# Kernel tuning notes

Measured on AMD Instinct MI355X. Metric: run time of the kernel, lower is better.

## Reference

```python
import jax, jax.numpy as jnp
import numpy as np

NUM_SEQS = 32      # decode batch: one new token per sequence
HIDDEN = 4096
H = 32             # query heads
KVH = 8            # kv heads (GQA group = 4)
D = 128            # head_dim
BS = 16            # paged-cache block size (vLLM default)
MAX_BLOCKS = 128   # blocks per sequence -> max context 2048
MAX_CTX = MAX_BLOCKS * BS
NUM_BLOCKS = NUM_SEQS * MAX_BLOCKS  # total physical blocks
ROPE_BASE = 10000.0


def setup_inputs() -> dict:
    key = jax.random.key(0)
    ks = jax.random.split(key, 10)
    s = 0.02
    hidden_states = jax.random.normal(ks[0], (NUM_SEQS, HIDDEN), jnp.float32)
    Wq = jax.random.normal(ks[1], (HIDDEN, H * D), jnp.float32) * s
    Wk = jax.random.normal(ks[2], (HIDDEN, KVH * D), jnp.float32) * s
    Wv = jax.random.normal(ks[3], (HIDDEN, KVH * D), jnp.float32) * s
    Wo = jax.random.normal(ks[4], (H * D, HIDDEN), jnp.float32) * s
    k_cache = jax.random.normal(ks[5], (NUM_BLOCKS, BS, KVH, D), jnp.float32)
    v_cache = jax.random.normal(ks[6], (NUM_BLOCKS, BS, KVH, D), jnp.float32)
    # disjoint, shuffled physical blocks per sequence (non-contiguous paging)
    perm = jax.random.permutation(ks[7], NUM_BLOCKS)
    block_tables = perm.reshape(NUM_SEQS, MAX_BLOCKS).astype(jnp.int32)
    context_lens = jax.random.randint(ks[8], (NUM_SEQS,), 1, MAX_CTX + 1).astype(jnp.int32)
    return dict(hidden_states=hidden_states, Wq=Wq, Wk=Wk, Wv=Wv, Wo=Wo,
                k_cache=k_cache, v_cache=v_cache,
                block_tables=block_tables, context_lens=context_lens)


def _rotate_half(x):
    x1, x2 = jnp.split(x, 2, axis=-1)
    return jnp.concatenate([-x2, x1], axis=-1)


def reference(hidden_states, Wq, Wk, Wv, Wo, k_cache, v_cache, block_tables, context_lens):
    T = hidden_states.shape[0]
    scale = D ** -0.5
    group = H // KVH

    # QKV projections
    q = (hidden_states @ Wq).reshape(T, H, D)
    k = (hidden_states @ Wk).reshape(T, KVH, D)
    v = (hidden_states @ Wv).reshape(T, KVH, D)

    # RoPE at position = context_len - 1 (HF half-split convention)
    pos = (context_lens - 1).astype(jnp.float32)
    inv_freq = 1.0 / (ROPE_BASE ** (jnp.arange(0, D, 2, dtype=jnp.float32) / D))
    freqs = pos[:, None] * inv_freq[None, :]                     # [T, D/2]
    cos = jnp.concatenate([jnp.cos(freqs)] * 2, -1)[:, None, :]  # [T, 1, D]
    sin = jnp.concatenate([jnp.sin(freqs)] * 2, -1)[:, None, :]
    q = q * cos + _rotate_half(q) * sin
    k = k * cos + _rotate_half(k) * sin

    # write new K/V into the paged cache at slot (ctx-1)
    last = context_lens - 1
    blk_idx = last // BS
    slot = last % BS
    phys = block_tables[jnp.arange(T), blk_idx]                  # [T]
    k_cache = k_cache.at[phys, slot].set(k)
    v_cache = v_cache.at[phys, slot].set(v)

    # gather each sequence's pages: [T, S, KVH, D], S = MAX_CTX
    K = k_cache[block_tables].reshape(T, MAX_CTX, KVH, D)
    V = v_cache[block_tables].reshape(T, MAX_CTX, KVH, D)

    # GQA attention, q_len = 1 per sequence
    qg = q.reshape(T, KVH, group, D)
    scores = jnp.einsum('tkgd,tskd->tkgs', qg, K) * scale        # [T, KVH, G, S]
    valid = jnp.arange(MAX_CTX)[None, :] < context_lens[:, None] # [T, S]
    scores = jnp.where(valid[:, None, None, :], scores, -jnp.inf)
    p = jax.nn.softmax(scores, axis=-1)
    out = jnp.einsum('tkgs,tskd->tkgd', p, V).reshape(T, H * D)
    return out @ Wo
```

## Files before the change

### kernel.cpp

```cpp
#include <hip/hip_runtime.h>
#include <math.h>

#define TSEQ 32
#define HID  4096
#define NH   32
#define NKVH 8
#define HD   128
#define NCOL 6144
#define BSZ  16
#define MAXBLK 128
#define CH   256

#define N_PART   (32*32*6144)
#define OFF_Q    (N_PART)
#define OFF_KN   (OFF_Q  + 131072)
#define OFF_VN   (OFF_KN + 32768)
#define OFF_AT   (OFF_VN + 32768)
#define OFF_AP   (OFF_AT + 131072)
#define OFF_TAB  (OFF_AP + 133120)

__global__ __launch_bounds__(256) void rope_table(const int* __restrict__ ctxl,
                                                  float* __restrict__ tab) {
  int idx = blockIdx.x * 256 + threadIdx.x;
  if (idx >= 32 * 64) return;
  int t = idx >> 6, i = idx & 63;
  double pos = (double)(ctxl[t] - 1);
  double inv = exp(-(double)i * (9.210340371976184 / 64.0));
  double f = pos * inv;
  tab[idx * 2]     = (float)cos(f);
  tab[idx * 2 + 1] = (float)sin(f);
}

__global__ __launch_bounds__(256) void qkv_kernel(
    const float* __restrict__ hs, const float* __restrict__ Wq,
    const float* __restrict__ Wk, const float* __restrict__ Wv,
    float* __restrict__ part) {
  const int lane = threadIdx.x & 63;
  const int wu = __builtin_amdgcn_readfirstlane(threadIdx.x >> 6);
  const int col0 = blockIdx.x * 256 + lane * 4;
  const int kc = blockIdx.y;
  const int k0 = kc * 128;
  const float* W; int ldw, jloc;
  if (col0 < 4096)      { W = Wq; ldw = 4096; jloc = col0; }
  else if (col0 < 5120) { W = Wk; ldw = 1024; jloc = col0 - 4096; }
  else                  { W = Wv; ldw = 1024; jloc = col0 - 5120; }
  float4 acc[8];
#pragma unroll
  for (int r = 0; r < 8; ++r) acc[r] = make_float4(0.f, 0.f, 0.f, 0.f);
  const float* wp = W + (size_t)k0 * ldw + jloc;
  const float* hp = hs + (size_t)(wu * 8) * HID + k0;
#pragma unroll 4
  for (int kk = 0; kk < 128; ++kk) {
    float4 w4 = *(const float4*)(wp + (size_t)kk * ldw);
#pragma unroll
    for (int r = 0; r < 8; ++r) {
      float h = hp[r * HID + kk];
      acc[r].x = fmaf(h, w4.x, acc[r].x);
      acc[r].y = fmaf(h, w4.y, acc[r].y);
      acc[r].z = fmaf(h, w4.z, acc[r].z);
      acc[r].w = fmaf(h, w4.w, acc[r].w);
    }
  }
  float* o = part + (size_t)kc * 32 * NCOL + (size_t)(wu * 8) * NCOL + blockIdx.x * 256 + lane * 4;
#pragma unroll
  for (int r = 0; r < 8; ++r) *(float4*)(o + (size_t)r * NCOL) = acc[r];
}

__global__ __launch_bounds__(256) void rope_kernel(
    const float* __restrict__ part, const float* __restrict__ tab,
    float* __restrict__ q, float* __restrict__ kn, float* __restrict__ vn) {
  const int t = blockIdx.x;
  const int col = (blockIdx.y * 256 + threadIdx.x) * 4;
  float4 sum = make_float4(0.f, 0.f, 0.f, 0.f);
  const float* p = part + (size_t)t * NCOL + col;
#pragma unroll
  for (int c = 0; c < 32; ++c) {
    float4 v = *(const float4*)(p + (size_t)c * 32 * NCOL);
    sum.x += v.x; sum.y += v.y; sum.z += v.z; sum.w += v.w;
  }
  __shared__ float lds[1024];
  *(float4*)&lds[threadIdx.x * 4] = sum;
  __syncthreads();
  float out[4] = {sum.x, sum.y, sum.z, sum.w};
  if (col < 5120) {
#pragma unroll
    for (int j = 0; j < 4; ++j) {
      int d = (col + j) & 127;
      int i = d & 63;
      float partner = lds[(threadIdx.x * 4 + j) ^ 64];
      float c0 = tab[(t * 64 + i) * 2];
      float s0 = tab[(t * 64 + i) * 2 + 1];
      out[j] = (d < 64) ? (out[j] * c0 - partner * s0) : (out[j] * c0 + partner * s0);
    }
  }
  float4 o4 = make_float4(out[0], out[1], out[2], out[3]);
  if (col < 4096)      *(float4*)(q  + (size_t)t * 4096 + col) = o4;
  else if (col < 5120) *(float4*)(kn + (size_t)t * 1024 + (col - 4096)) = o4;
  else                 *(float4*)(vn + (size_t)t * 1024 + (col - 5120)) = o4;
}

__global__ __launch_bounds__(256) void attn_kernel(
    const float* __restrict__ kcache, const float* __restrict__ vcache,
    const int* __restrict__ bt, const int* __restrict__ ctxl,
    const float* __restrict__ q, const float* __restrict__ kn,
    const float* __restrict__ vn, float* __restrict__ part) {
  const int t = blockIdx.x, kvh = blockIdx.y, ch = blockIdx.z;
  const int ctx = ctxl[t];
  const int s0 = ch * CH;
  if (s0 >= ctx) return;
  const int ns = min(CH, ctx - s0);
  const int tid = threadIdx.x;
  const int w = tid >> 6, lane = tid & 63;
  const int half = lane >> 5, dl = lane & 31;

  __shared__ float qs[4][128];
  __shared__ int   bts[128];
  __shared__ float sc[4][CH];
  __shared__ float ml[4][2];
  __shared__ float op[4][4][128];

  for (int i = tid; i < 512; i += 256)
    qs[i >> 7][i & 127] = q[((size_t)t * NH + kvh * 4 + (i >> 7)) * HD + (i & 127)];
  for (int i = tid; i < 128; i += 256) bts[i] = bt[t * MAXBLK + i];
  __syncthreads();

  float4 q0 = *(const float4*)(&qs[0][dl * 4]);
  float4 q1 = *(const float4*)(&qs[1][dl * 4]);
  float4 q2 = *(const float4*)(&qs[2][dl * 4]);
  float4 q3 = *(const float4*)(&qs[3][dl * 4]);
  const float* knp = kn + ((size_t)t * NKVH + kvh) * HD;
  const float* vnp = vn + ((size_t)t * NKVH + kvh) * HD;

#pragma unroll 2
  for (int i = 0; i < CH / 8; ++i) {
    int sl = i * 8 + w * 2 + half;
    bool valid = sl < ns;
    float dot0 = 0.f, dot1 = 0.f, dot2 = 0.f, dot3 = 0.f;
    if (valid) {
      int s = s0 + sl;
      const float* kp;
      if (s == ctx - 1) kp = knp;
      else {
        int phys = bts[s >> 4];
        kp = kcache + (((size_t)phys * BSZ + (s & 15)) * NKVH + kvh) * HD;
      }
      float4 k4 = *(const float4*)(kp + dl * 4);
      dot0 = q0.x*k4.x + q0.y*k4.y + q0.z*k4.z + q0.w*k4.w;
      dot1 = q1.x*k4.x + q1.y*k4.y + q1.z*k4.z + q1.w*k4.w;
      dot2 = q2.x*k4.x + q2.y*k4.y + q2.z*k4.z + q2.w*k4.w;
      dot3 = q3.x*k4.x + q3.y*k4.y + q3.z*k4.z + q3.w*k4.w;
    }
#pragma unroll
    for (int m = 1; m < 32; m <<= 1) {
      dot0 += __shfl_xor(dot0, m, 64);
      dot1 += __shfl_xor(dot1, m, 64);
      dot2 += __shfl_xor(dot2, m, 64);
      dot3 += __shfl_xor(dot3, m, 64);
    }
    if (dl == 0) {
      const float scale = 0.08838834764831845f;
      sc[0][sl] = valid ? dot0 * scale : -INFINITY;
      sc[1][sl] = valid ? dot1 * scale : -INFINITY;
      sc[2][sl] = valid ? dot2 * scale : -INFINITY;
      sc[3][sl] = valid ? dot3 * scale : -INFINITY;
    }
  }
  __syncthreads();

  {
    const int g = w;
    float vals[4];
    float m = -INFINITY;
#pragma unroll
    for (int i = 0; i < 4; ++i) { vals[i] = sc[g][lane + i * 64]; m = fmaxf(m, vals[i]); }
#pragma unroll
    for (int mk = 1; mk < 64; mk <<= 1) m = fmaxf(m, __shfl_xor(m, mk, 64));
    float l = 0.f;
#pragma unroll
    for (int i = 0; i < 4; ++i) {
      float pv = __expf(vals[i] - m);
      sc[g][lane + i * 64] = pv;
      l += pv;
    }
#pragma unroll
    for (int mk = 1; mk < 64; mk <<= 1) l += __shfl_xor(l, mk, 64);
    if (lane == 0) { ml[g][0] = m; ml[g][1] = l; }
  }
  __syncthreads();

  {
    float acc[4][4];
#pragma unroll
    for (int g = 0; g < 4; ++g)
#pragma unroll
      for (int j = 0; j < 4; ++j) acc[g][j] = 0.f;
    const int base = w * 64;
#pragma unroll 2
    for (int i = 0; i < 32; ++i) {
      int sl = base + i * 2 + half;
      if (sl < ns) {
        int s = s0 + sl;
        const float* vp;
        if (s == ctx - 1) vp = vnp;
        else {
          int phys = bts[s >> 4];
          vp = vcache + (((size_t)phys * BSZ + (s & 15)) * NKVH + kvh) * HD;
        }
        float4 v4 = *(const float4*)(vp + dl * 4);
        float p0 = sc[0][sl], p1 = sc[1][sl], p2 = sc[2][sl], p3 = sc[3][sl];
        acc[0][0] = fmaf(p0, v4.x, acc[0][0]); acc[0][1] = fmaf(p0, v4.y, acc[0][1]);
        acc[0][2] = fmaf(p0, v4.z, acc[0][2]); acc[0][3] = fmaf(p0, v4.w, acc[0][3]);
        acc[1][0] = fmaf(p1, v4.x, acc[1][0]); acc[1][1] = fmaf(p1, v4.y, acc[1][1]);
        acc[1][2] = fmaf(p1, v4.z, acc[1][2]); acc[1][3] = fmaf(p1, v4.w, acc[1][3]);
        acc[2][0] = fmaf(p2, v4.x, acc[2][0]); acc[2][1] = fmaf(p2, v4.y, acc[2][1]);
        acc[2][2] = fmaf(p2, v4.z, acc[2][2]); acc[2][3] = fmaf(p2, v4.w, acc[2][3]);
        acc[3][0] = fmaf(p3, v4.x, acc[3][0]); acc[3][1] = fmaf(p3, v4.y, acc[3][1]);
        acc[3][2] = fmaf(p3, v4.z, acc[3][2]); acc[3][3] = fmaf(p3, v4.w, acc[3][3]);
      }
    }
#pragma unroll
    for (int g = 0; g < 4; ++g)
#pragma unroll
      for (int j = 0; j < 4; ++j) acc[g][j] += __shfl_xor(acc[g][j], 32, 64);
    if (half == 0) {
#pragma unroll
      for (int g = 0; g < 4; ++g)
        *(float4*)&op[w][g][dl * 4] = make_float4(acc[g][0], acc[g][1], acc[g][2], acc[g][3]);
    }
  }
  __syncthreads();

  float* pp = part + ((size_t)(t * NKVH + kvh) * 8 + ch) * 520;
  for (int j = tid; j < 512; j += 256) {
    int g = j >> 7, d = j & 127;
    pp[8 + g * 128 + d] = op[0][g][d] + op[1][g][d] + op[2][g][d] + op[3][g][d];
  }
  if (tid < 4) { pp[tid] = ml[tid][0]; pp[4 + tid] = ml[tid][1]; }
}

__global__ __launch_bounds__(128) void combine_kernel(
    const float* __restrict__ part, const int* __restrict__ ctxl,
    float* __restrict__ attn) {
  const int t = blockIdx.x, kvh = blockIdx.y;
  const int nc = (ctxl[t] + CH - 1) / CH;
  const int d = threadIdx.x;
#pragma unroll
  for (int g = 0; g < 4; ++g) {
    float m = -INFINITY;
    for (int c = 0; c < nc; ++c)
      m = fmaxf(m, part[((size_t)(t * NKVH + kvh) * 8 + c) * 520 + g]);
    float l = 0.f, o = 0.f;
    for (int c = 0; c < nc; ++c) {
      const float* pp = part + ((size_t)(t * NKVH + kvh) * 8 + c) * 520;
      float scl = __expf(pp[g] - m);
      l += pp[4 + g] * scl;
      o += pp[8 + g * 128 + d] * scl;
    }
    attn[((size_t)t * NH + kvh * 4 + g) * HD + d] = o / l;
  }
}

__global__ __launch_bounds__(256) void proj_kernel(
    const float* __restrict__ attn, const float* __restrict__ Wo,
    float* __restrict__ part) {
  const int lane = threadIdx.x & 63;
  const int wu = __builtin_amdgcn_readfirstlane(threadIdx.x >> 6);
  const int col0 = blockIdx.x * 256 + lane * 4;
  const int kc = blockIdx.y;
  const int k0 = kc * 128;
  float4 acc[8];
#pragma unroll
  for (int r = 0; r < 8; ++r) acc[r] = make_float4(0.f, 0.f, 0.f, 0.f);
  const float* wp = Wo + (size_t)k0 * 4096 + col0;
  const float* hp = attn + (size_t)(wu * 8) * 4096 + k0;
#pragma unroll 4
  for (int kk = 0; kk < 128; ++kk) {
    float4 w4 = *(const float4*)(wp + (size_t)kk * 4096);
#pragma unroll
    for (int r = 0; r < 8; ++r) {
      float h = hp[r * 4096 + kk];
      acc[r].x = fmaf(h, w4.x, acc[r].x);
      acc[r].y = fmaf(h, w4.y, acc[r].y);
      acc[r].z = fmaf(h, w4.z, acc[r].z);
      acc[r].w = fmaf(h, w4.w, acc[r].w);
    }
  }
  float* o = part + (size_t)kc * 32 * 4096 + (size_t)(wu * 8) * 4096 + blockIdx.x * 256 + lane * 4;
#pragma unroll
  for (int r = 0; r < 8; ++r) *(float4*)(o + (size_t)r * 4096) = acc[r];
}

__global__ __launch_bounds__(256) void reduce_out(
    const float* __restrict__ part, float* __restrict__ out) {
  const int t = blockIdx.x;
  const int col = (blockIdx.y * 256 + threadIdx.x) * 4;
  float4 s0 = make_float4(0.f,0.f,0.f,0.f), s1 = make_float4(0.f,0.f,0.f,0.f);
  const float* p = part + (size_t)t * 4096 + col;
#pragma unroll
  for (int c = 0; c < 32; c += 2) {
    float4 a = *(const float4*)(p + (size_t)c * 32 * 4096);
    float4 b = *(const float4*)(p + (size_t)(c + 1) * 32 * 4096);
    s0.x += a.x; s0.y += a.y; s0.z += a.z; s0.w += a.w;
    s1.x += b.x; s1.y += b.y; s1.z += b.z; s1.w += b.w;
  }
  float4 s = make_float4(s0.x + s1.x, s0.y + s1.y, s0.z + s1.z, s0.w + s1.w);
  *(float4*)(out + (size_t)t * 4096 + col) = s;
}

extern "C" void kernel_launch(void* const* d_in, const int* in_sizes, int n_in,
                              void* d_out, int out_size, void* d_ws, size_t ws_size,
                              hipStream_t stream) {
  const float* hs = (const float*)d_in[0];
  const float* Wq = (const float*)d_in[1];
  const float* Wk = (const float*)d_in[2];
  const float* Wv = (const float*)d_in[3];
  const float* Wo = (const float*)d_in[4];
  const float* kc = (const float*)d_in[5];
  const float* vc = (const float*)d_in[6];
  const int*   bt = (const int*)d_in[7];
  const int*   cl = (const int*)d_in[8];
  float* out = (float*)d_out;
  float* ws  = (float*)d_ws;

  float* part = ws;
  float* q    = ws + OFF_Q;
  float* kn   = ws + OFF_KN;
  float* vn   = ws + OFF_VN;
  float* at   = ws + OFF_AT;
  float* ap   = ws + OFF_AP;
  float* tab  = ws + OFF_TAB;

  rope_table<<<dim3(8), 256, 0, stream>>>(cl, tab);
  qkv_kernel<<<dim3(24, 32), 256, 0, stream>>>(hs, Wq, Wk, Wv, part);
  rope_kernel<<<dim3(32, 6), 256, 0, stream>>>(part, tab, q, kn, vn);
  attn_kernel<<<dim3(32, 8, 8), 256, 0, stream>>>(kc, vc, bt, cl, q, kn, vn, ap);
  combine_kernel<<<dim3(32, 8), 128, 0, stream>>>(ap, cl, at);
  proj_kernel<<<dim3(16, 32), 256, 0, stream>>>(at, Wo, part);
  reduce_out<<<dim3(32, 4), 256, 0, stream>>>(part, out);
}
```

Baseline: 189.2 us.

## Restructure attention to thread-per-token scoring, halve GEMM split-K, fuse RoPE table

Attention now gives each thread a full token: it computes four group dot products over all 128 dims serially, runs the softmax max/sum inside each wave, and combines the per-wave partials with rescaling. This removes the per-token shuffle reductions and one barrier pass. The QKV and output GEMMs use 16 K-chunks of 256 with 512-thread blocks, which shrinks partial-sum traffic and the reduce work. The RoPE table kernel is folded into the rope kernel, saving a launch. The trade-off is that per-thread K loads are now strided across lanes (uncoalesced, 512B stride), which may hurt memory efficiency.

```diff
diff --git a/kernel.cpp b/kernel.cpp
--- a/kernel.cpp
+++ b/kernel.cpp
@@ -10,28 +10,16 @@
 #define BSZ  16
 #define MAXBLK 128
 #define CH   256
-
-#define N_PART   (32*32*6144)
+#define NKC  16
+
+#define N_PART   (NKC*32*6144)
 #define OFF_Q    (N_PART)
 #define OFF_KN   (OFF_Q  + 131072)
 #define OFF_VN   (OFF_KN + 32768)
 #define OFF_AT   (OFF_VN + 32768)
 #define OFF_AP   (OFF_AT + 131072)
-#define OFF_TAB  (OFF_AP + 133120)
-
-__global__ __launch_bounds__(256) void rope_table(const int* __restrict__ ctxl,
-                                                  float* __restrict__ tab) {
-  int idx = blockIdx.x * 256 + threadIdx.x;
-  if (idx >= 32 * 64) return;
-  int t = idx >> 6, i = idx & 63;
-  double pos = (double)(ctxl[t] - 1);
-  double inv = exp(-(double)i * (9.210340371976184 / 64.0));
-  double f = pos * inv;
-  tab[idx * 2]     = (float)cos(f);
-  tab[idx * 2 + 1] = (float)sin(f);
-}
-
-__global__ __launch_bounds__(256) void qkv_kernel(
+
+__global__ __launch_bounds__(512) void qkv_kernel(
     const float* __restrict__ hs, const float* __restrict__ Wq,
     const float* __restrict__ Wk, const float* __restrict__ Wv,
     float* __restrict__ part) {
@@ -39,21 +27,21 @@
   const int wu = __builtin_amdgcn_readfirstlane(threadIdx.x >> 6);
   const int col0 = blockIdx.x * 256 + lane * 4;
   const int kc = blockIdx.y;
-  const int k0 = kc * 128;
+  const int k0 = kc * 256;
   const float* W; int ldw, jloc;
   if (col0 < 4096)      { W = Wq; ldw = 4096; jloc = col0; }
   else if (col0 < 5120) { W = Wk; ldw = 1024; jloc = col0 - 4096; }
   else                  { W = Wv; ldw = 1024; jloc = col0 - 5120; }
-  float4 acc[8];
-#pragma unroll
-  for (int r = 0; r < 8; ++r) acc[r] = make_float4(0.f, 0.f, 0.f, 0.f);
+  float4 acc[4];
+#pragma unroll
+  for (int r = 0; r < 4; ++r) acc[r] = make_float4(0.f, 0.f, 0.f, 0.f);
   const float* wp = W + (size_t)k0 * ldw + jloc;
-  const float* hp = hs + (size_t)(wu * 8) * HID + k0;
+  const float* hp = hs + (size_t)(wu * 4) * HID + k0;
 #pragma unroll 4
-  for (int kk = 0; kk < 128; ++kk) {
+  for (int kk = 0; kk < 256; ++kk) {
     float4 w4 = *(const float4*)(wp + (size_t)kk * ldw);
 #pragma unroll
-    for (int r = 0; r < 8; ++r) {
+    for (int r = 0; r < 4; ++r) {
       float h = hp[r * HID + kk];
       acc[r].x = fmaf(h, w4.x, acc[r].x);
       acc[r].y = fmaf(h, w4.y, acc[r].y);
@@ -61,25 +49,33 @@
       acc[r].w = fmaf(h, w4.w, acc[r].w);
     }
   }
-  float* o = part + (size_t)kc * 32 * NCOL + (size_t)(wu * 8) * NCOL + blockIdx.x * 256 + lane * 4;
-#pragma unroll
-  for (int r = 0; r < 8; ++r) *(float4*)(o + (size_t)r * NCOL) = acc[r];
+  float* o = part + (size_t)kc * 32 * NCOL + (size_t)(wu * 4) * NCOL + blockIdx.x * 256 + lane * 4;
+#pragma unroll
+  for (int r = 0; r < 4; ++r) *(float4*)(o + (size_t)r * NCOL) = acc[r];
 }
 
 __global__ __launch_bounds__(256) void rope_kernel(
-    const float* __restrict__ part, const float* __restrict__ tab,
+    const float* __restrict__ part, const int* __restrict__ ctxl,
     float* __restrict__ q, float* __restrict__ kn, float* __restrict__ vn) {
   const int t = blockIdx.x;
   const int col = (blockIdx.y * 256 + threadIdx.x) * 4;
   float4 sum = make_float4(0.f, 0.f, 0.f, 0.f);
   const float* p = part + (size_t)t * NCOL + col;
 #pragma unroll
-  for (int c = 0; c < 32; ++c) {
+  for (int c = 0; c < NKC; ++c) {
     float4 v = *(const float4*)(p + (size_t)c * 32 * NCOL);
     sum.x += v.x; sum.y += v.y; sum.z += v.z; sum.w += v.w;
   }
   __shared__ float lds[1024];
+  __shared__ float tcs[64], tsn[64];
   *(float4*)&lds[threadIdx.x * 4] = sum;
+  if (threadIdx.x < 64) {
+    double pos = (double)(ctxl[t] - 1);
+    double inv = exp(-(double)threadIdx.x * (9.210340371976184 / 64.0));
+    double f = pos * inv;
+    tcs[threadIdx.x] = (float)cos(f);
+    tsn[threadIdx.x] = (float)sin(f);
+  }
   __syncthreads();
   float out[4] = {sum.x, sum.y, sum.z, sum.w};
   if (col < 5120) {
@@ -88,8 +84,7 @@
       int d = (col + j) & 127;
       int i = d & 63;
       float partner = lds[(threadIdx.x * 4 + j) ^ 64];
-      float c0 = tab[(t * 64 + i) * 2];
-      float s0 = tab[(t * 64 + i) * 2 + 1];
+      float c0 = tcs[i], s0 = tsn[i];
       out[j] = (d < 64) ? (out[j] * c0 - partner * s0) : (out[j] * c0 + partner * s0);
     }
   }
@@ -111,131 +106,119 @@
   const int ns = min(CH, ctx - s0);
   const int tid = threadIdx.x;
   const int w = tid >> 6, lane = tid & 63;
-  const int half = lane >> 5, dl = lane & 31;
 
   __shared__ float qs[4][128];
-  __shared__ int   bts[128];
-  __shared__ float sc[4][CH];
-  __shared__ float ml[4][2];
-  __shared__ float op[4][4][128];
+  __shared__ int   bts[16];
+  __shared__ float pl[4][64][4];
+  __shared__ float om[4][4], ol[4][4];
+  __shared__ float oacc[4][4][128];
 
   for (int i = tid; i < 512; i += 256)
     qs[i >> 7][i & 127] = q[((size_t)t * NH + kvh * 4 + (i >> 7)) * HD + (i & 127)];
-  for (int i = tid; i < 128; i += 256) bts[i] = bt[t * MAXBLK + i];
+  if (tid < 16) bts[tid] = bt[t * MAXBLK + ch * 16 + tid];
   __syncthreads();
 
-  float4 q0 = *(const float4*)(&qs[0][dl * 4]);
-  float4 q1 = *(const float4*)(&qs[1][dl * 4]);
-  float4 q2 = *(const float4*)(&qs[2][dl * 4]);
-  float4 q3 = *(const float4*)(&qs[3][dl * 4]);
   const float* knp = kn + ((size_t)t * NKVH + kvh) * HD;
   const float* vnp = vn + ((size_t)t * NKVH + kvh) * HD;
 
-#pragma unroll 2
-  for (int i = 0; i < CH / 8; ++i) {
-    int sl = i * 8 + w * 2 + half;
-    bool valid = sl < ns;
-    float dot0 = 0.f, dot1 = 0.f, dot2 = 0.f, dot3 = 0.f;
-    if (valid) {
-      int s = s0 + sl;
-      const float* kp;
-      if (s == ctx - 1) kp = knp;
-      else {
-        int phys = bts[s >> 4];
-        kp = kcache + (((size_t)phys * BSZ + (s & 15)) * NKVH + kvh) * HD;
-      }
-      float4 k4 = *(const float4*)(kp + dl * 4);
-      dot0 = q0.x*k4.x + q0.y*k4.y + q0.z*k4.z + q0.w*k4.w;
-      dot1 = q1.x*k4.x + q1.y*k4.y + q1.z*k4.z + q1.w*k4.w;
-      dot2 = q2.x*k4.x + q2.y*k4.y + q2.z*k4.z + q2.w*k4.w;
-      dot3 = q3.x*k4.x + q3.y*k4.y + q3.z*k4.z + q3.w*k4.w;
-    }
-#pragma unroll
-    for (int m = 1; m < 32; m <<= 1) {
-      dot0 += __shfl_xor(dot0, m, 64);
-      dot1 += __shfl_xor(dot1, m, 64);
-      dot2 += __shfl_xor(dot2, m, 64);
-      dot3 += __shfl_xor(dot3, m, 64);
-    }
-    if (dl == 0) {
-      const float scale = 0.08838834764831845f;
-      sc[0][sl] = valid ? dot0 * scale : -INFINITY;
-      sc[1][sl] = valid ? dot1 * scale : -INFINITY;
-      sc[2][sl] = valid ? dot2 * scale : -INFINITY;
-      sc[3][sl] = valid ? dot3 * scale : -INFINITY;
-    }
-  }
+  const int sl = w * 64 + lane;
+  const int s  = s0 + sl;
+  const bool valid = sl < ns;
+  const float* kp;
+  {
+    int phys = bts[sl >> 4];
+    const float* kreal = kcache + (((size_t)phys * BSZ + (sl & 15)) * NKVH + kvh) * HD;
+    kp = (!valid || s == ctx - 1) ? knp : kreal;
+  }
+  float dot0 = 0.f, dot1 = 0.f, dot2 = 0.f, dot3 = 0.f;
+#pragma unroll 8
+  for (int d0 = 0; d0 < 128; d0 += 4) {
+    float4 k4 = *(const float4*)(kp + d0);
+    float4 q0 = *(const float4*)(&qs[0][d0]);
+    float4 q1 = *(const float4*)(&qs[1][d0]);
+    float4 q2 = *(const float4*)(&qs[2][d0]);
+    float4 q3 = *(const float4*)(&qs[3][d0]);
+    dot0 = fmaf(q0.x,k4.x,fmaf(q0.y,k4.y,fmaf(q0.z,k4.z,fmaf(q0.w,k4.w,dot0))));
+    dot1 = fmaf(q1.x,k4.x,fmaf(q1.y,k4.y,fmaf(q1.z,k4.z,fmaf(q1.w,k4.w,dot1))));
+    dot2 = fmaf(q2.x,k4.x,fmaf(q2.y,k4.y,fmaf(q2.z,k4.z,fmaf(q2.w,k4.w,dot2))));
+    dot3 = fmaf(q3.x,k4.x,fmaf(q3.y,k4.y,fmaf(q3.z,k4.z,fmaf(q3.w,k4.w,dot3))));
+  }
+  const float scale = 0.08838834764831845f;
+  float sc0 = valid ? dot0 * scale : -INFINITY;
+  float sc1 = valid ? dot1 * scale : -INFINITY;
+  float sc2 = valid ? dot2 * scale : -INFINITY;
+  float sc3 = valid ? dot3 * scale : -INFINITY;
+
+  float m0 = sc0, m1 = sc1, m2 = sc2, m3 = sc3;
+#pragma unroll
+  for (int mk = 1; mk < 64; mk <<= 1) {
+    m0 = fmaxf(m0, __shfl_xor(m0, mk, 64));
+    m1 = fmaxf(m1, __shfl_xor(m1, mk, 64));
+    m2 = fmaxf(m2, __shfl_xor(m2, mk, 64));
+    m3 = fmaxf(m3, __shfl_xor(m3, mk, 64));
+  }
+  float p0 = __expf(sc0 - fmaxf(m0, -3e38f));
+  float p1 = __expf(sc1 - fmaxf(m1, -3e38f));
+  float p2 = __expf(sc2 - fmaxf(m2, -3e38f));
+  float p3 = __expf(sc3 - fmaxf(m3, -3e38f));
+  float l0 = p0, l1 = p1, l2 = p2, l3 = p3;
+#pragma unroll
+  for (int mk = 1; mk < 64; mk <<= 1) {
+    l0 += __shfl_xor(l0, mk, 64);
+    l1 += __shfl_xor(l1, mk, 64);
+    l2 += __shfl_xor(l2, mk, 64);
+    l3 += __shfl_xor(l3, mk, 64);
+  }
+  *(float4*)&pl[w][lane][0] = make_float4(p0, p1, p2, p3);
+  if (lane == 0) {
+    om[w][0] = m0; om[w][1] = m1; om[w][2] = m2; om[w][3] = m3;
+    ol[w][0] = l0; ol[w][1] = l1; ol[w][2] = l2; ol[w][3] = l3;
+  }
+
+  float a00=0.f,a01=0.f,a10=0.f,a11=0.f,a20=0.f,a21=0.f,a30=0.f,a31=0.f;
+  int nsw = ns - w * 64; nsw = nsw < 0 ? 0 : (nsw > 64 ? 64 : nsw);
+  for (int b4 = 0; b4 < 4; ++b4) {
+    int base = b4 * 16;
+    if (base >= nsw) break;
+    int phys = bts[w * 4 + b4];
+    const float* vbase = vcache + (((size_t)phys * BSZ) * NKVH + kvh) * HD;
+    int jmax = min(16, nsw - base);
+#pragma unroll 4
+    for (int j = 0; j < jmax; ++j) {
+      int s2 = s0 + w * 64 + base + j;
+      const float* vp = (s2 == ctx - 1) ? vnp : vbase + (size_t)j * NKVH * HD;
+      float2 v2 = *(const float2*)(vp + lane * 2);
+      float4 p4 = *(const float4*)&pl[w][base + j][0];
+      a00 = fmaf(p4.x, v2.x, a00); a01 = fmaf(p4.x, v2.y, a01);
+      a10 = fmaf(p4.y, v2.x, a10); a11 = fmaf(p4.y, v2.y, a11);
+      a20 = fmaf(p4.z, v2.x, a20); a21 = fmaf(p4.z, v2.y, a21);
+      a30 = fmaf(p4.w, v2.x, a30); a31 = fmaf(p4.w, v2.y, a31);
+    }
+  }
+  *(float2*)&oacc[w][0][lane * 2] = make_float2(a00, a01);
+  *(float2*)&oacc[w][1][lane * 2] = make_float2(a10, a11);
+  *(float2*)&oacc[w][2][lane * 2] = make_float2(a20, a21);
+  *(float2*)&oacc[w][3][lane * 2] = make_float2(a30, a31);
   __syncthreads();
 
+  float* pp = part + ((size_t)(t * NKVH + kvh) * 8 + ch) * 520;
   {
-    const int g = w;
-    float vals[4];
-    float m = -INFINITY;
-#pragma unroll
-    for (int i = 0; i < 4; ++i) { vals[i] = sc[g][lane + i * 64]; m = fmaxf(m, vals[i]); }
-#pragma unroll
-    for (int mk = 1; mk < 64; mk <<= 1) m = fmaxf(m, __shfl_xor(m, mk, 64));
-    float l = 0.f;
-#pragma unroll
-    for (int i = 0; i < 4; ++i) {
-      float pv = __expf(vals[i] - m);
-      sc[g][lane + i * 64] = pv;
-      l += pv;
-    }
-#pragma unroll
-    for (int mk = 1; mk < 64; mk <<= 1) l += __shfl_xor(l, mk, 64);
-    if (lane == 0) { ml[g][0] = m; ml[g][1] = l; }
-  }
-  __syncthreads();
-
-  {
-    float acc[4][4];
-#pragma unroll
-    for (int g = 0; g < 4; ++g)
-#pragma unroll
-      for (int j = 0; j < 4; ++j) acc[g][j] = 0.f;
-    const int base = w * 64;
-#pragma unroll 2
-    for (int i = 0; i < 32; ++i) {
-      int sl = base + i * 2 + half;
-      if (sl < ns) {
-        int s = s0 + sl;
-        const float* vp;
-        if (s == ctx - 1) vp = vnp;
-        else {
-          int phys = bts[s >> 4];
-          vp = vcache + (((size_t)phys * BSZ + (s & 15)) * NKVH + kvh) * HD;
-        }
-        float4 v4 = *(const float4*)(vp + dl * 4);
-        float p0 = sc[0][sl], p1 = sc[1][sl], p2 = sc[2][sl], p3 = sc[3][sl];
-        acc[0][0] = fmaf(p0, v4.x, acc[0][0]); acc[0][1] = fmaf(p0, v4.y, acc[0][1]);
-        acc[0][2] = fmaf(p0, v4.z, acc[0][2]); acc[0][3] = fmaf(p0, v4.w, acc[0][3]);
-        acc[1][0] = fmaf(p1, v4.x, acc[1][0]); acc[1][1] = fmaf(p1, v4.y, acc[1][1]);
-        acc[1][2] = fmaf(p1, v4.z, acc[1][2]); acc[1][3] = fmaf(p1, v4.w, acc[1][3]);
-        acc[2][0] = fmaf(p2, v4.x, acc[2][0]); acc[2][1] = fmaf(p2, v4.y, acc[2][1]);
-        acc[2][2] = fmaf(p2, v4.z, acc[2][2]); acc[2][3] = fmaf(p2, v4.w, acc[2][3]);
-        acc[3][0] = fmaf(p3, v4.x, acc[3][0]); acc[3][1] = fmaf(p3, v4.y, acc[3][1]);
-        acc[3][2] = fmaf(p3, v4.z, acc[3][2]); acc[3][3] = fmaf(p3, v4.w, acc[3][3]);
-      }
-    }
-#pragma unroll
-    for (int g = 0; g < 4; ++g)
-#pragma unroll
-      for (int j = 0; j < 4; ++j) acc[g][j] += __shfl_xor(acc[g][j], 32, 64);
-    if (half == 0) {
-#pragma unroll
-      for (int g = 0; g < 4; ++g)
-        *(float4*)&op[w][g][dl * 4] = make_float4(acc[g][0], acc[g][1], acc[g][2], acc[g][3]);
-    }
-  }
-  __syncthreads();
-
-  float* pp = part + ((size_t)(t * NKVH + kvh) * 8 + ch) * 520;
-  for (int j = tid; j < 512; j += 256) {
-    int g = j >> 7, d = j & 127;
-    pp[8 + g * 128 + d] = op[0][g][d] + op[1][g][d] + op[2][g][d] + op[3][g][d];
-  }
-  if (tid < 4) { pp[tid] = ml[tid][0]; pp[4 + tid] = ml[tid][1]; }
+    const int g = tid >> 6, d0 = (tid & 63) * 2;
+    float mw0 = om[0][g], mw1 = om[1][g], mw2 = om[2][g], mw3 = om[3][g];
+    float M = fmaxf(fmaxf(mw0, mw1), fmaxf(mw2, mw3));
+    float Ms = fmaxf(M, -3e38f);
+    float e0 = __expf(fmaxf(mw0, -3e38f) - Ms);
+    float e1 = __expf(fmaxf(mw1, -3e38f) - Ms);
+    float e2 = __expf(fmaxf(mw2, -3e38f) - Ms);
+    float e3 = __expf(fmaxf(mw3, -3e38f) - Ms);
+    float ox = e0*oacc[0][g][d0]   + e1*oacc[1][g][d0]   + e2*oacc[2][g][d0]   + e3*oacc[3][g][d0];
+    float oy = e0*oacc[0][g][d0+1] + e1*oacc[1][g][d0+1] + e2*oacc[2][g][d0+1] + e3*oacc[3][g][d0+1];
+    *(float2*)(pp + 8 + g * 128 + d0) = make_float2(ox, oy);
+    if ((tid & 63) == 0) {
+      pp[g]     = M;
+      pp[4 + g] = e0*ol[0][g] + e1*ol[1][g] + e2*ol[2][g] + e3*ol[3][g];
+    }
+  }
 }
 
 __global__ __launch_bounds__(128) void combine_kernel(
@@ -260,24 +243,24 @@
   }
 }
 
-__global__ __launch_bounds__(256) void proj_kernel(
+__global__ __launch_bounds__(512) void proj_kernel(
     const float* __restrict__ attn, const float* __restrict__ Wo,
     float* __restrict__ part) {
   const int lane = threadIdx.x & 63;
   const int wu = __builtin_amdgcn_readfirstlane(threadIdx.x >> 6);
   const int col0 = blockIdx.x * 256 + lane * 4;
   const int kc = blockIdx.y;
-  const int k0 = kc * 128;
-  float4 acc[8];
-#pragma unroll
-  for (int r = 0; r < 8; ++r) acc[r] = make_float4(0.f, 0.f, 0.f, 0.f);
+  const int k0 = kc * 256;
+  float4 acc[4];
+#pragma unroll
+  for (int r = 0; r < 4; ++r) acc[r] = make_float4(0.f, 0.f, 0.f, 0.f);
   const float* wp = Wo + (size_t)k0 * 4096 + col0;
-  const float* hp = attn + (size_t)(wu * 8) * 4096 + k0;
+  const float* hp = attn + (size_t)(wu * 4) * 4096 + k0;
 #pragma unroll 4
-  for (int kk = 0; kk < 128; ++kk) {
+  for (int kk = 0; kk < 256; ++kk) {
     float4 w4 = *(const float4*)(wp + (size_t)kk * 4096);
 #pragma unroll
-    for (int r = 0; r < 8; ++r) {
+    for (int r = 0; r < 4; ++r) {
       float h = hp[r * 4096 + kk];
       acc[r].x = fmaf(h, w4.x, acc[r].x);
       acc[r].y = fmaf(h, w4.y, acc[r].y);
@@ -285,9 +268,9 @@
       acc[r].w = fmaf(h, w4.w, acc[r].w);
     }
   }
-  float* o = part + (size_t)kc * 32 * 4096 + (size_t)(wu * 8) * 4096 + blockIdx.x * 256 + lane * 4;
-#pragma unroll
-  for (int r = 0; r < 8; ++r) *(float4*)(o + (size_t)r * 4096) = acc[r];
+  float* o = part + (size_t)kc * 32 * 4096 + (size_t)(wu * 4) * 4096 + blockIdx.x * 256 + lane * 4;
+#pragma unroll
+  for (int r = 0; r < 4; ++r) *(float4*)(o + (size_t)r * 4096) = acc[r];
 }
 
 __global__ __launch_bounds__(256) void reduce_out(
@@ -297,7 +280,7 @@
   float4 s0 = make_float4(0.f,0.f,0.f,0.f), s1 = make_float4(0.f,0.f,0.f,0.f);
   const float* p = part + (size_t)t * 4096 + col;
 #pragma unroll
-  for (int c = 0; c < 32; c += 2) {
+  for (int c = 0; c < NKC; c += 2) {
     float4 a = *(const float4*)(p + (size_t)c * 32 * 4096);
     float4 b = *(const float4*)(p + (size_t)(c + 1) * 32 * 4096);
     s0.x += a.x; s0.y += a.y; s0.z += a.z; s0.w += a.w;
@@ -328,13 +311,11 @@
   float* vn   = ws + OFF_VN;
   float* at   = ws + OFF_AT;
   float* ap   = ws + OFF_AP;
-  float* tab  = ws + OFF_TAB;
-
-  rope_table<<<dim3(8), 256, 0, stream>>>(cl, tab);
-  qkv_kernel<<<dim3(24, 32), 256, 0, stream>>>(hs, Wq, Wk, Wv, part);
-  rope_kernel<<<dim3(32, 6), 256, 0, stream>>>(part, tab, q, kn, vn);
+
+  qkv_kernel<<<dim3(24, NKC), 512, 0, stream>>>(hs, Wq, Wk, Wv, part);
+  rope_kernel<<<dim3(32, 6), 256, 0, stream>>>(part, cl, q, kn, vn);
   attn_kernel<<<dim3(32, 8, 8), 256, 0, stream>>>(kc, vc, bt, cl, q, kn, vn, ap);
   combine_kernel<<<dim3(32, 8), 128, 0, stream>>>(ap, cl, at);
-  proj_kernel<<<dim3(16, 32), 256, 0, stream>>>(at, Wo, part);
+  proj_kernel<<<dim3(16, NKC), 512, 0, stream>>>(at, Wo, part);
   reduce_out<<<dim3(32, 4), 256, 0, stream>>>(part, out);
 }
```

New measurement: 198.5 us. 1.05x slower.
